# Kernel optimization log

Hardware: AMD Instinct MI355X
Metric: run time of the kernel (lower is better)

The kernel has to match this reference:

```python
import jax, jax.numpy as jnp
import numpy as np

NEG_FILL = -1.0e9
PROB_MIN = 1e-9


def _lstm_cell(x, h, c, w_ih, w_hh, b_ih, b_hh):
    # PyTorch gate order: input, forget, cell(g), output
    gates = x @ w_ih.T + h @ w_hh.T + b_ih + b_hh
    i, f, g, o = jnp.split(gates, 4, axis=-1)
    c_new = jax.nn.sigmoid(f) * c + jax.nn.sigmoid(i) * jnp.tanh(g)
    h_new = jax.nn.sigmoid(o) * jnp.tanh(c_new)
    return h_new, c_new


def setup_inputs() -> dict:
    key = jax.random.key(0)
    B, T, D, H, W = 2048, 100, 128, 256, 256
    ks = jax.random.split(key, 16)
    s_d = 1.0 / np.sqrt(D)
    s_h = 1.0 / np.sqrt(H)
    s_w = 1.0 / np.sqrt(W)
    return {
        "targets": jax.random.normal(ks[0], (B, T, D), jnp.float32),
        "h0": jax.random.normal(ks[1], (1, B, H), jnp.float32),
        "c0": jax.random.normal(ks[2], (1, B, H), jnp.float32),
        "enc_w_ih": jax.random.normal(ks[3], (4 * H, D), jnp.float32) * s_d,
        "enc_w_hh": jax.random.normal(ks[4], (4 * H, H), jnp.float32) * s_h,
        "enc_b_ih": jax.random.normal(ks[5], (4 * H,), jnp.float32) * s_h,
        "enc_b_hh": jax.random.normal(ks[6], (4 * H,), jnp.float32) * s_h,
        "dec_w_ih": jax.random.normal(ks[7], (4 * H, D), jnp.float32) * s_d,
        "dec_w_hh": jax.random.normal(ks[8], (4 * H, H), jnp.float32) * s_h,
        "dec_b_ih": jax.random.normal(ks[9], (4 * H,), jnp.float32) * s_h,
        "dec_b_hh": jax.random.normal(ks[10], (4 * H,), jnp.float32) * s_h,
        "W1": jax.random.normal(ks[11], (W, H), jnp.float32) * s_h,
        "W2": jax.random.normal(ks[12], (W, H), jnp.float32) * s_h,
        "vt": jax.random.normal(ks[13], (W,), jnp.float32) * s_w,
    }


def reference(targets, h0, c0, enc_w_ih, enc_w_hh, enc_b_ih, enc_b_hh,
              dec_w_ih, dec_w_hh, dec_b_ih, dec_b_hh, W1, W2, vt):
    B, T, D = targets.shape
    H = enc_w_hh.shape[1]

    # ---- encoder LSTM (batch_first, zero initial state) ----
    def enc_step(carry, x_t):
        h, c = carry
        h, c = _lstm_cell(x_t, h, c, enc_w_ih, enc_w_hh, enc_b_ih, enc_b_hh)
        return (h, c), h

    z = jnp.zeros((B, H), targets.dtype)
    _, enc_h = jax.lax.scan(enc_step, (z, z), jnp.swapaxes(targets, 0, 1))
    encoder_states = jnp.swapaxes(enc_h, 0, 1)  # [B, T, H]

    blend1 = encoder_states @ W1.T  # [B, T, W]

    a1 = jnp.arange(B)
    init = (h0[0], c0[0], jnp.zeros((B, T), dtype=bool), jnp.zeros_like(targets[:, 0]))

    def dec_step(carry, _):
        h, c, selected, dec_in = carry
        h, c = _lstm_cell(dec_in, h, c, dec_w_ih, dec_w_hh, dec_b_ih, dec_b_hh)
        blend2 = h @ W2.T                                   # [B, W]
        scores = jnp.tanh(blend1 + blend2[:, None, :]) @ vt  # [B, T]
        scores = jnp.where(selected, NEG_FILL, scores)
        sel = jnp.argmax(scores, axis=-1)                    # [B]
        selected = selected.at[a1, sel].set(True)
        probs = jnp.maximum(jax.nn.softmax(scores, axis=-1), PROB_MIN)
        dec_in = targets[a1, sel]                            # [B, D]
        return (h, c, selected, dec_in), probs

    _, probs = jax.lax.scan(dec_step, init, None, length=T)
    return jnp.swapaxes(probs, 0, 1)  # [B, T, T]
```

## Files before the change

### kernel.cpp

```cpp
#include <hip/hip_runtime.h>
#include <math.h>
#include <stdint.h>

#define BB 2048
#define TT 100
#define DD 128
#define HH 256
#define NEGF -1.0e9f

#define NBLK 128
#define ROWS 16
#define NTHR 512
#define KTOT 384
#define NKF  12
#define ASTR 392

typedef __attribute__((ext_vector_type(8))) short short8_t;
typedef __attribute__((ext_vector_type(4))) float f32x4;

#define MFMA16(a,b,c) __builtin_amdgcn_mfma_f32_16x16x32_bf16((a),(b),(c),0,0,0)
#define MFMA_X6(aH,aM,aL,bH,bM,bL,acc)            \
  do{ acc = MFMA16(aM, bM, acc);                  \
      acc = MFMA16(aH, bL, acc);                  \
      acc = MFMA16(aL, bH, acc);                  \
      acc = MFMA16(aH, bM, acc);                  \
      acc = MFMA16(aM, bH, acc);                  \
      acc = MFMA16(aH, bH, acc); }while(0)

__device__ __forceinline__ float sigmoidf_(float x){ return 1.0f/(1.0f+expf(-x)); }

__device__ __forceinline__ float tanh_fast(float x){
  x = fminf(15.f, fmaxf(-15.f, x));
  const float e = __expf(x + x);
  return (e - 1.f) * __builtin_amdgcn_rcpf(e + 1.f);
}

__device__ __forceinline__ void bf16_split3(float x, unsigned short &h,
                                            unsigned short &m, unsigned short &l){
  const unsigned u = __float_as_uint(x);
  const unsigned r = u + 0x7FFFu + ((u >> 16) & 1u);
  h = (unsigned short)(r >> 16);
  const float rem = x - __uint_as_float(r & 0xFFFF0000u);
  const unsigned u2 = __float_as_uint(rem);
  const unsigned r2 = u2 + 0x7FFFu + ((u2 >> 16) & 1u);
  m = (unsigned short)(r2 >> 16);
  const float rem2 = rem - __uint_as_float(r2 & 0xFFFF0000u);
  l = (unsigned short)(__float_as_uint(rem2) >> 16);
}

__global__ __launch_bounds__(256) void k_split3(const float* __restrict__ src,
    unsigned short* __restrict__ hi, unsigned short* __restrict__ mi,
    unsigned short* __restrict__ lo, int n){
  const int i = blockIdx.x*256 + threadIdx.x;
  if(i < n){ unsigned short h,m,l; bf16_split3(src[i], h, m, l);
             hi[i]=h; mi[i]=m; lo[i]=l; }
}

__global__ __launch_bounds__(256) void k_transpose256(const float* __restrict__ in,
                                                      float* __restrict__ outp){
  const int k = blockIdx.x;
  const int n = threadIdx.x;
  outp[k*256 + n] = in[n*256 + k];
}

__global__ __launch_bounds__(256) void k_packW(
    const float* __restrict__ w_ih, const float* __restrict__ w_hh,
    unsigned short* __restrict__ WfH, unsigned short* __restrict__ WfM,
    unsigned short* __restrict__ WfL)
{
  const int i = blockIdx.x*256 + threadIdx.x;
  if(i >= 1024*KTOT) return;
  const int f    = i / (NKF*64*8);
  const int r1   = i % (NKF*64*8);
  const int kf   = r1 >> 9;
  const int r2   = r1 & 511;
  const int lane = r2 >> 3;
  const int e    = r2 & 7;
  const int n = f*16 + (lane & 15);
  const int k = kf*32 + (lane >> 4)*8 + e;
  const float w = (k < DD) ? w_ih[(size_t)n*DD + k] : w_hh[(size_t)n*HH + (k-DD)];
  unsigned short h,m,l; bf16_split3(w,h,m,l);
  WfH[i]=h; WfM[i]=m; WfL[i]=l;
}

__device__ __forceinline__ int swA(int row, int byteoff){
  return row*ASTR + (((byteoff) ^ ((row & 7) << 4)) >> 1);
}

__global__ __launch_bounds__(NTHR) void k_encoder(
    const float* __restrict__ targets,
    const unsigned short* __restrict__ WfH, const unsigned short* __restrict__ WfM,
    const unsigned short* __restrict__ WfL,
    const float* __restrict__ bih, const float* __restrict__ bhh,
    float* __restrict__ blend1)
{
  __shared__ unsigned short AsH[ROWS*ASTR], AsM[ROWS*ASTR], AsL[ROWS*ASTR];
  const int tid = threadIdx.x;
  const int lane = tid & 63;
  const int wv = tid >> 6;
  const int l15 = lane & 15, l4 = lane >> 4;
  const int b0 = blockIdx.x * ROWS;

  float bias[8];
  #pragma unroll
  for(int g=0; g<4; g++)
    #pragma unroll
    for(int c16=0; c16<2; c16++){
      const int n = g*256 + wv*32 + c16*16 + l15;
      bias[g*2+c16] = bih[n] + bhh[n];
    }
  float cst[2][4];
  #pragma unroll
  for(int a=0;a<2;a++)
    #pragma unroll
    for(int r=0;r<4;r++) cst[a][r] = 0.f;

  for(int i=tid; i<ROWS*ASTR; i+=NTHR){ AsH[i]=0; AsM[i]=0; AsL[i]=0; }

  const int srow = tid >> 5;
  const int k4   = (tid & 31) * 4;
  const int sidx = swA(srow, k4*2);

  for(int t=0; t<TT; t++){
    __syncthreads();
    {
      const float4 v = *(const float4*)(targets + ((size_t)(b0+srow)*TT + t)*DD + k4);
      unsigned short h0,m0_,l0,h1,m1_,l1,h2,m2_,l2,h3,m3_,l3;
      bf16_split3(v.x,h0,m0_,l0); bf16_split3(v.y,h1,m1_,l1);
      bf16_split3(v.z,h2,m2_,l2); bf16_split3(v.w,h3,m3_,l3);
      *(ushort4*)&AsH[sidx] = make_ushort4(h0,h1,h2,h3);
      *(ushort4*)&AsM[sidx] = make_ushort4(m0_,m1_,m2_,m3_);
      *(ushort4*)&AsL[sidx] = make_ushort4(l0,l1,l2,l3);
    }
    __syncthreads();
    f32x4 acc[8];
    #pragma unroll
    for(int ff=0; ff<8; ff++){
      acc[ff][0]=bias[ff]; acc[ff][1]=bias[ff]; acc[ff][2]=bias[ff]; acc[ff][3]=bias[ff];
    }
    for(int kf=0; kf<NKF; kf++){
      const int ao = swA(l15, kf*64 + l4*16);
      const short8_t aH = *(const short8_t*)&AsH[ao];
      const short8_t aM = *(const short8_t*)&AsM[ao];
      const short8_t aL = *(const short8_t*)&AsL[ao];
      #pragma unroll
      for(int g=0; g<4; g++)
        #pragma unroll
        for(int c16=0; c16<2; c16++){
          const int f = g*16 + wv*2 + c16;
          const size_t wo = ((size_t)(f*NKF + kf)*64 + lane)*8;
          const short8_t bH = *(const short8_t*)(WfH + wo);
          const short8_t bM = *(const short8_t*)(WfM + wo);
          const short8_t bL = *(const short8_t*)(WfL + wo);
          MFMA_X6(aH,aM,aL,bH,bM,bL, acc[g*2+c16]);
        }
    }
    __syncthreads();
    #pragma unroll
    for(int c16=0; c16<2; c16++){
      const int j = wv*32 + c16*16 + l15;
      #pragma unroll
      for(int r=0; r<4; r++){
        const int row = l4*4 + r;
        const float iv = acc[0+c16][r];
        const float fv = acc[2+c16][r];
        const float gv = acc[4+c16][r];
        const float ov = acc[6+c16][r];
        const float cn = sigmoidf_(fv)*cst[c16][r] + sigmoidf_(iv)*tanhf(gv);
        const float hn = sigmoidf_(ov)*tanhf(cn);
        cst[c16][r] = cn;
        unsigned short sh, sm_, sl;
        bf16_split3(hn, sh, sm_, sl);
        const int hi = swA(row, (128 + j)*2);
        AsH[hi] = sh; AsM[hi] = sm_; AsL[hi] = sl;
        blend1[((size_t)(b0+row)*TT + t)*256 + j] = hn;
      }
    }
  }
}

__global__ __launch_bounds__(NTHR) void k_decoder(
    const float* __restrict__ targets,
    const unsigned short* __restrict__ WfH, const unsigned short* __restrict__ WfM,
    const unsigned short* __restrict__ WfL,
    const float* __restrict__ bih, const float* __restrict__ bhh,
    const float* __restrict__ h0, const float* __restrict__ c0,
    const float* __restrict__ W2t, const float* __restrict__ vt,
    const float* __restrict__ blend1,
    float* __restrict__ outp)
{
  __shared__ unsigned short AsH[ROWS*ASTR], AsM[ROWS*ASTR], AsL[ROWS*ASTR];
  __shared__ float hs[ROWS*264];
  __shared__ float b2s[ROWS*264];
  __shared__ float sc[ROWS][104];
  __shared__ float vts[256];
  __shared__ char selc[ROWS][104];
  const int tid = threadIdx.x;
  const int lane = tid & 63;
  const int wv = tid >> 6;
  const int l15 = lane & 15, l4 = lane >> 4;
  const int b0 = blockIdx.x * ROWS;

  float bias[8];
  #pragma unroll
  for(int g=0; g<4; g++)
    #pragma unroll
    for(int c16=0; c16<2; c16++){
      const int n = g*256 + wv*32 + c16*16 + l15;
      bias[g*2+c16] = bih[n] + bhh[n];
    }

  for(int i=tid; i<ROWS*ASTR; i+=NTHR){ AsH[i]=0; AsM[i]=0; AsL[i]=0; }
  if(tid < 256) vts[tid] = vt[tid];
  for(int i=tid; i<ROWS*104; i+=NTHR) (&selc[0][0])[i] = 0;
  {
    const int row = tid >> 5;
    const int k8  = (tid & 31) * 8;
    #pragma unroll
    for(int ii=0; ii<8; ii+=4){
      const float4 v = *(const float4*)(h0 + (size_t)(b0+row)*HH + k8 + ii);
      unsigned short h0_,m0_,l0,h1,m1_,l1,h2,m2_,l2,h3,m3_,l3;
      bf16_split3(v.x,h0_,m0_,l0); bf16_split3(v.y,h1,m1_,l1);
      bf16_split3(v.z,h2,m2_,l2); bf16_split3(v.w,h3,m3_,l3);
      const int idx = swA(row, (128 + k8 + ii)*2);
      *(ushort4*)&AsH[idx] = make_ushort4(h0_,h1,h2,h3);
      *(ushort4*)&AsM[idx] = make_ushort4(m0_,m1_,m2_,m3_);
      *(ushort4*)&AsL[idx] = make_ushort4(l0,l1,l2,l3);
    }
  }
  float cst[2][4];
  #pragma unroll
  for(int c16=0; c16<2; c16++)
    #pragma unroll
    for(int r=0; r<4; r++)
      cst[c16][r] = c0[(size_t)(b0 + l4*4 + r)*HH + wv*32 + c16*16 + l15];

  for(int st=0; st<TT; st++){
    __syncthreads();
    f32x4 acc[8];
    #pragma unroll
    for(int ff=0; ff<8; ff++){
      acc[ff][0]=bias[ff]; acc[ff][1]=bias[ff]; acc[ff][2]=bias[ff]; acc[ff][3]=bias[ff];
    }
    for(int kf=0; kf<NKF; kf++){
      const int ao = swA(l15, kf*64 + l4*16);
      const short8_t aH = *(const short8_t*)&AsH[ao];
      const short8_t aM = *(const short8_t*)&AsM[ao];
      const short8_t aL = *(const short8_t*)&AsL[ao];
      #pragma unroll
      for(int g=0; g<4; g++)
        #pragma unroll
        for(int c16=0; c16<2; c16++){
          const int f = g*16 + wv*2 + c16;
          const size_t wo = ((size_t)(f*NKF + kf)*64 + lane)*8;
          const short8_t bH = *(const short8_t*)(WfH + wo);
          const short8_t bM = *(const short8_t*)(WfM + wo);
          const short8_t bL = *(const short8_t*)(WfL + wo);
          MFMA_X6(aH,aM,aL,bH,bM,bL, acc[g*2+c16]);
        }
    }
    __syncthreads();
    #pragma unroll
    for(int c16=0; c16<2; c16++){
      const int j = wv*32 + c16*16 + l15;
      #pragma unroll
      for(int r=0; r<4; r++){
        const int row = l4*4 + r;
        const float iv = acc[0+c16][r];
        const float fv = acc[2+c16][r];
        const float gv = acc[4+c16][r];
        const float ov = acc[6+c16][r];
        const float cn = sigmoidf_(fv)*cst[c16][r] + sigmoidf_(iv)*tanhf(gv);
        const float hn = sigmoidf_(ov)*tanhf(cn);
        cst[c16][r] = cn;
        unsigned short sh, sm_, sl;
        bf16_split3(hn, sh, sm_, sl);
        const int hi = swA(row, (128 + j)*2);
        AsH[hi] = sh; AsM[hi] = sm_; AsL[hi] = sl;
        hs[row*264 + j] = hn;
      }
    }
    __syncthreads();
    {
      const int row = tid >> 5;
      const int n8  = (tid & 31) * 8;
      float a8[8];
      #pragma unroll
      for(int i=0;i<8;i++) a8[i] = 0.f;
      #pragma unroll 4
      for(int k=0; k<HH; k++){
        const float hv = hs[row*264 + k];
        const float4 w0 = *(const float4*)(W2t + (size_t)k*HH + n8);
        const float4 w1 = *(const float4*)(W2t + (size_t)k*HH + n8 + 4);
        a8[0]=fmaf(hv,w0.x,a8[0]); a8[1]=fmaf(hv,w0.y,a8[1]);
        a8[2]=fmaf(hv,w0.z,a8[2]); a8[3]=fmaf(hv,w0.w,a8[3]);
        a8[4]=fmaf(hv,w1.x,a8[4]); a8[5]=fmaf(hv,w1.y,a8[5]);
        a8[6]=fmaf(hv,w1.z,a8[6]); a8[7]=fmaf(hv,w1.w,a8[7]);
      }
      #pragma unroll
      for(int i=0;i<8;i++) b2s[row*264 + n8 + i] = a8[i];
    }
    __syncthreads();
    {
      const int g4 = lane >> 4, l16 = lane & 15;
      #pragma unroll
      for(int rr=0; rr<2; rr++){
        const int row = wv*2 + rr;
        const float* bl  = blend1 + ((size_t)(b0+row)*TT)*256;
        const float* b2p = &b2s[row*264];
        for(int tb=0; tb<25; tb++){
          const int t = tb*4 + g4;
          float p = 0.f;
          #pragma unroll
          for(int q=0; q<4; q++){
            const int k = l16*16 + q*4;
            const float4 x   = *(const float4*)(bl + (size_t)t*256 + k);
            const float4 b2v = *(const float4*)(b2p + k);
            const float4 vv4 = *(const float4*)(&vts[k]);
            p = fmaf(tanh_fast(x.x + b2v.x), vv4.x, p);
            p = fmaf(tanh_fast(x.y + b2v.y), vv4.y, p);
            p = fmaf(tanh_fast(x.z + b2v.z), vv4.z, p);
            p = fmaf(tanh_fast(x.w + b2v.w), vv4.w, p);
          }
          #pragma unroll
          for(int off=8; off>=1; off>>=1) p += __shfl_xor(p, off, 64);
          if(l16 == 0) sc[row][t] = p;
        }
      }
    }
    __syncthreads();
    #pragma unroll
    for(int rr=0; rr<2; rr++){
      const int row  = wv*2 + rr;
      const int brow = b0 + row;
      const float m1 = selc[row][lane] ? NEGF : sc[row][lane];
      float bestv = m1; int besti = lane;
      const int t2 = lane + 64;
      float m2 = NEGF;
      if(t2 < TT){
        m2 = selc[row][t2] ? NEGF : sc[row][t2];
        if(m2 > bestv){ bestv = m2; besti = t2; }
      }
      #pragma unroll
      for(int off=32; off>=1; off>>=1){
        const float ov = __shfl_xor(bestv, off, 64);
        const int   oi = __shfl_xor(besti, off, 64);
        if(ov > bestv || (ov == bestv && oi < besti)){ bestv = ov; besti = oi; }
      }
      float e = __expf(m1 - bestv);
      if(t2 < TT) e += __expf(m2 - bestv);
      #pragma unroll
      for(int off=32; off>=1; off>>=1) e += __shfl_xor(e, off, 64);

      float* orow = outp + (size_t)brow*(TT*TT) + (size_t)st*TT;
      orow[lane] = fmaxf(__expf(m1 - bestv)/e, 1e-9f);
      if(t2 < TT) orow[t2] = fmaxf(__expf(m2 - bestv)/e, 1e-9f);
      if(lane == 0) selc[row][besti] = 1;
      #pragma unroll
      for(int dd=0; dd<2; dd++){
        const int d = lane + dd*64;
        const float xv = targets[((size_t)brow*TT + besti)*DD + d];
        unsigned short th, tm, tl;
        bf16_split3(xv, th, tm, tl);
        const int idx = swA(row, d*2);
        AsH[idx] = th; AsM[idx] = tm; AsL[idx] = tl;
      }
    }
  }
}

__global__ __launch_bounds__(128) void k_blend1(
    float* __restrict__ blend1,
    const unsigned short* __restrict__ W1H, const unsigned short* __restrict__ W1M,
    const unsigned short* __restrict__ W1L)
{
  __shared__ alignas(16) unsigned short AsH[32*264], AsM[32*264], AsL[32*264];
  const int tid  = threadIdx.x;
  const int lane = tid & 63;
  const int wv   = tid >> 6;
  const int l15  = lane & 15;
  const int l4   = lane >> 4;
  const size_t r0 = (size_t)blockIdx.x * 32;

  #pragma unroll
  for(int it=0; it<16; it++){
    const int q  = it*128 + tid;
    const int r  = q >> 6;
    const int kq = (q & 63) << 2;
    const float4 v = *(const float4*)(blend1 + (r0+r)*256 + kq);
    unsigned short h0,m0_,l0,h1,m1_,l1,h2,m2_,l2,h3,m3_,l3;
    bf16_split3(v.x,h0,m0_,l0); bf16_split3(v.y,h1,m1_,l1);
    bf16_split3(v.z,h2,m2_,l2); bf16_split3(v.w,h3,m3_,l3);
    *(ushort4*)&AsH[r*264+kq] = make_ushort4(h0,h1,h2,h3);
    *(ushort4*)&AsM[r*264+kq] = make_ushort4(m0_,m1_,m2_,m3_);
    *(ushort4*)&AsL[r*264+kq] = make_ushort4(l0,l1,l2,l3);
  }
  __syncthreads();

  f32x4 acc[16];
  #pragma unroll
  for(int s=0;s<16;s++)
    #pragma unroll
    for(int e=0;e<4;e++) acc[s][e] = 0.f;

  const int rb = wv*16;
  for(int kt=0; kt<8; kt++){
    const int k0 = kt*32;
    const short8_t aH = *(const short8_t*)&AsH[(rb+l15)*264 + k0 + l4*8];
    const short8_t aM = *(const short8_t*)&AsM[(rb+l15)*264 + k0 + l4*8];
    const short8_t aL = *(const short8_t*)&AsL[(rb+l15)*264 + k0 + l4*8];
    #pragma unroll
    for(int fn=0; fn<16; fn++){
      const int n = fn*16 + l15;
      const short8_t bH = *(const short8_t*)(W1H + (size_t)n*256 + k0 + l4*8);
      const short8_t bM = *(const short8_t*)(W1M + (size_t)n*256 + k0 + l4*8);
      const short8_t bL = *(const short8_t*)(W1L + (size_t)n*256 + k0 + l4*8);
      MFMA_X6(aH,aM,aL, bH,bM,bL, acc[fn]);
    }
  }
  #pragma unroll
  for(int fn=0; fn<16; fn++)
    #pragma unroll
    for(int r=0; r<4; r++)
      blend1[(r0 + rb + l4*4 + r)*256 + fn*16 + l15] = acc[fn][r];
}

extern "C" void kernel_launch(void* const* d_in, const int* in_sizes, int n_in,
                              void* d_out, int out_size, void* d_ws, size_t ws_size,
                              hipStream_t stream)
{
  (void)in_sizes; (void)n_in; (void)out_size; (void)ws_size;
  const float* targets  = (const float*)d_in[0];
  const float* h0       = (const float*)d_in[1];
  const float* c0       = (const float*)d_in[2];
  const float* enc_w_ih = (const float*)d_in[3];
  const float* enc_w_hh = (const float*)d_in[4];
  const float* enc_b_ih = (const float*)d_in[5];
  const float* enc_b_hh = (const float*)d_in[6];
  const float* dec_w_ih = (const float*)d_in[7];
  const float* dec_w_hh = (const float*)d_in[8];
  const float* dec_b_ih = (const float*)d_in[9];
  const float* dec_b_hh = (const float*)d_in[10];
  const float* W1       = (const float*)d_in[11];
  const float* W2       = (const float*)d_in[12];
  const float* vt       = (const float*)d_in[13];
  float* outp = (float*)d_out;

  float* ws      = (float*)d_ws;
  float* blend1  = ws;
  float* W2t     = blend1 + (size_t)BB*TT*256;
  char* pc = (char*)(W2t + 256*256);
  pc = (char*)(((uintptr_t)pc + 63) & ~(uintptr_t)63);
  unsigned short* q = (unsigned short*)pc;
  const size_t WFSZ = (size_t)1024*KTOT;
  unsigned short* eWfH = q; q += WFSZ;
  unsigned short* eWfM = q; q += WFSZ;
  unsigned short* eWfL = q; q += WFSZ;
  unsigned short* dWfH = q; q += WFSZ;
  unsigned short* dWfM = q; q += WFSZ;
  unsigned short* dWfL = q; q += WFSZ;
  unsigned short* w1H  = q; q += (size_t)256*256;
  unsigned short* w1M  = q; q += (size_t)256*256;
  unsigned short* w1L  = q; q += (size_t)256*256;

  const int packGrid = (1024*KTOT + 255)/256;
  k_packW<<<packGrid, 256, 0, stream>>>(enc_w_ih, enc_w_hh, eWfH, eWfM, eWfL);
  k_packW<<<packGrid, 256, 0, stream>>>(dec_w_ih, dec_w_hh, dWfH, dWfM, dWfL);
  k_split3<<<(256*256+255)/256, 256, 0, stream>>>(W1, w1H, w1M, w1L, 256*256);
  k_transpose256<<<256, 256, 0, stream>>>(W2, W2t);

  k_encoder<<<NBLK, NTHR, 0, stream>>>(targets, eWfH, eWfM, eWfL,
                                       enc_b_ih, enc_b_hh, blend1);

  k_blend1<<<BB*TT/32, 128, 0, stream>>>(blend1, w1H, w1M, w1L);

  k_decoder<<<NBLK, NTHR, 0, stream>>>(targets, dWfH, dWfM, dWfL,
                                       dec_b_ih, dec_b_hh, h0, c0,
                                       W2t, vt, blend1, outp);
}
```

Measured before the change: 15.94 ms.

## Spread LSTM recurrences over more blocks and move decoder W2 projection to MFMA

The decoder now handles 8 batch rows per block across 256 blocks with 1024 threads, padding the MFMA A tile to 16 rows. The encoder keeps 16 rows per block but uses 1024 threads, so each wave owns one 16-column slice per gate. The scalar fp32 h@W2 loop is replaced by a 3-way bf16-split MFMA against a prepacked W2, and output probabilities are written with nontemporal stores. The intent is to use more CUs and cut per-step latency on the serial recurrence. The cost is wasted MFMA work on the padded rows and more threads contending at each barrier.

```diff
diff --git a/kernel.cpp b/kernel.cpp
--- a/kernel.cpp
+++ b/kernel.cpp
@@ -8,9 +8,10 @@
 #define HH 256
 #define NEGF -1.0e9f
 
-#define NBLK 128
-#define ROWS 16
-#define NTHR 512
+#define NBLK 256
+#define ROWS 8
+#define RA   16
+#define NTHR 1024
 #define KTOT 384
 #define NKF  12
 #define ASTR 392
@@ -54,13 +55,6 @@
   const int i = blockIdx.x*256 + threadIdx.x;
   if(i < n){ unsigned short h,m,l; bf16_split3(src[i], h, m, l);
              hi[i]=h; mi[i]=m; lo[i]=l; }
-}
-
-__global__ __launch_bounds__(256) void k_transpose256(const float* __restrict__ in,
-                                                      float* __restrict__ outp){
-  const int k = blockIdx.x;
-  const int n = threadIdx.x;
-  outp[k*256 + n] = in[n*256 + k];
 }
 
 __global__ __launch_bounds__(256) void k_packW(
@@ -83,6 +77,25 @@
   WfH[i]=h; WfM[i]=m; WfL[i]=l;
 }
 
+__global__ __launch_bounds__(256) void k_packW2(
+    const float* __restrict__ W2,
+    unsigned short* __restrict__ WfH, unsigned short* __restrict__ WfM,
+    unsigned short* __restrict__ WfL)
+{
+  const int i = blockIdx.x*256 + threadIdx.x;
+  if(i >= 256*256) return;
+  const int f2   = i >> 12;
+  const int r1   = i & 4095;
+  const int kf2  = r1 >> 9;
+  const int r2   = r1 & 511;
+  const int lane = r2 >> 3;
+  const int e    = r2 & 7;
+  const int n = f2*16 + (lane & 15);
+  const int k = kf2*32 + (lane >> 4)*8 + e;
+  unsigned short h,m,l; bf16_split3(W2[(size_t)n*HH + k], h, m, l);
+  WfH[i]=h; WfM[i]=m; WfL[i]=l;
+}
+
 __device__ __forceinline__ int swA(int row, int byteoff){
   return row*ASTR + (((byteoff) ^ ((row & 7) << 4)) >> 1);
 }
@@ -94,49 +107,43 @@
     const float* __restrict__ bih, const float* __restrict__ bhh,
     float* __restrict__ blend1)
 {
-  __shared__ unsigned short AsH[ROWS*ASTR], AsM[ROWS*ASTR], AsL[ROWS*ASTR];
+  __shared__ unsigned short AsH[RA*ASTR], AsM[RA*ASTR], AsL[RA*ASTR];
   const int tid = threadIdx.x;
   const int lane = tid & 63;
   const int wv = tid >> 6;
   const int l15 = lane & 15, l4 = lane >> 4;
-  const int b0 = blockIdx.x * ROWS;
-
-  float bias[8];
-  #pragma unroll
-  for(int g=0; g<4; g++)
-    #pragma unroll
-    for(int c16=0; c16<2; c16++){
-      const int n = g*256 + wv*32 + c16*16 + l15;
-      bias[g*2+c16] = bih[n] + bhh[n];
-    }
-  float cst[2][4];
-  #pragma unroll
-  for(int a=0;a<2;a++)
-    #pragma unroll
-    for(int r=0;r<4;r++) cst[a][r] = 0.f;
-
-  for(int i=tid; i<ROWS*ASTR; i+=NTHR){ AsH[i]=0; AsM[i]=0; AsL[i]=0; }
-
-  const int srow = tid >> 5;
-  const int k4   = (tid & 31) * 4;
-  const int sidx = swA(srow, k4*2);
+  const int b0 = blockIdx.x * RA;
+
+  const int j = wv*16 + l15;
+  float bias[4];
+  #pragma unroll
+  for(int g=0; g<4; g++) bias[g] = bih[g*HH + j] + bhh[g*HH + j];
+
+  float cst[4];
+  #pragma unroll
+  for(int r=0;r<4;r++) cst[r] = 0.f;
+
+  for(int i=tid; i<RA*ASTR; i+=NTHR){ AsH[i]=0; AsM[i]=0; AsL[i]=0; }
+
+  const int srow = tid >> 6;
+  const int k2   = (tid & 63) * 2;
 
   for(int t=0; t<TT; t++){
     __syncthreads();
     {
-      const float4 v = *(const float4*)(targets + ((size_t)(b0+srow)*TT + t)*DD + k4);
-      unsigned short h0,m0_,l0,h1,m1_,l1,h2,m2_,l2,h3,m3_,l3;
+      const float2 v = *(const float2*)(targets + ((size_t)(b0+srow)*TT + t)*DD + k2);
+      unsigned short h0,m0_,l0,h1,m1_,l1;
       bf16_split3(v.x,h0,m0_,l0); bf16_split3(v.y,h1,m1_,l1);
-      bf16_split3(v.z,h2,m2_,l2); bf16_split3(v.w,h3,m3_,l3);
-      *(ushort4*)&AsH[sidx] = make_ushort4(h0,h1,h2,h3);
-      *(ushort4*)&AsM[sidx] = make_ushort4(m0_,m1_,m2_,m3_);
-      *(ushort4*)&AsL[sidx] = make_ushort4(l0,l1,l2,l3);
-    }
-    __syncthreads();
-    f32x4 acc[8];
-    #pragma unroll
-    for(int ff=0; ff<8; ff++){
-      acc[ff][0]=bias[ff]; acc[ff][1]=bias[ff]; acc[ff][2]=bias[ff]; acc[ff][3]=bias[ff];
+      const int idx = swA(srow, k2*2);
+      *(ushort2*)&AsH[idx] = make_ushort2(h0,h1);
+      *(ushort2*)&AsM[idx] = make_ushort2(m0_,m1_);
+      *(ushort2*)&AsL[idx] = make_ushort2(l0,l1);
+    }
+    __syncthreads();
+    f32x4 acc[4];
+    #pragma unroll
+    for(int g=0; g<4; g++){
+      acc[g][0]=bias[g]; acc[g][1]=bias[g]; acc[g][2]=bias[g]; acc[g][3]=bias[g];
     }
     for(int kf=0; kf<NKF; kf++){
       const int ao = swA(l15, kf*64 + l4*16);
@@ -144,37 +151,31 @@
       const short8_t aM = *(const short8_t*)&AsM[ao];
       const short8_t aL = *(const short8_t*)&AsL[ao];
       #pragma unroll
-      for(int g=0; g<4; g++)
-        #pragma unroll
-        for(int c16=0; c16<2; c16++){
-          const int f = g*16 + wv*2 + c16;
-          const size_t wo = ((size_t)(f*NKF + kf)*64 + lane)*8;
-          const short8_t bH = *(const short8_t*)(WfH + wo);
-          const short8_t bM = *(const short8_t*)(WfM + wo);
-          const short8_t bL = *(const short8_t*)(WfL + wo);
-          MFMA_X6(aH,aM,aL,bH,bM,bL, acc[g*2+c16]);
-        }
-    }
-    __syncthreads();
-    #pragma unroll
-    for(int c16=0; c16<2; c16++){
-      const int j = wv*32 + c16*16 + l15;
-      #pragma unroll
-      for(int r=0; r<4; r++){
-        const int row = l4*4 + r;
-        const float iv = acc[0+c16][r];
-        const float fv = acc[2+c16][r];
-        const float gv = acc[4+c16][r];
-        const float ov = acc[6+c16][r];
-        const float cn = sigmoidf_(fv)*cst[c16][r] + sigmoidf_(iv)*tanhf(gv);
-        const float hn = sigmoidf_(ov)*tanhf(cn);
-        cst[c16][r] = cn;
-        unsigned short sh, sm_, sl;
-        bf16_split3(hn, sh, sm_, sl);
-        const int hi = swA(row, (128 + j)*2);
-        AsH[hi] = sh; AsM[hi] = sm_; AsL[hi] = sl;
-        blend1[((size_t)(b0+row)*TT + t)*256 + j] = hn;
-      }
+      for(int g=0; g<4; g++){
+        const int f = g*16 + wv;
+        const size_t wo = ((size_t)(f*NKF + kf)*64 + lane)*8;
+        const short8_t bH = *(const short8_t*)(WfH + wo);
+        const short8_t bM = *(const short8_t*)(WfM + wo);
+        const short8_t bL = *(const short8_t*)(WfL + wo);
+        MFMA_X6(aH,aM,aL,bH,bM,bL, acc[g]);
+      }
+    }
+    __syncthreads();
+    #pragma unroll
+    for(int r=0; r<4; r++){
+      const int row = l4*4 + r;
+      const float iv = acc[0][r];
+      const float fv = acc[1][r];
+      const float gv = acc[2][r];
+      const float ov = acc[3][r];
+      const float cn = sigmoidf_(fv)*cst[r] + sigmoidf_(iv)*tanhf(gv);
+      const float hn = sigmoidf_(ov)*tanhf(cn);
+      cst[r] = cn;
+      unsigned short sh, sm_, sl;
+      bf16_split3(hn, sh, sm_, sl);
+      const int hi = swA(row, (128 + j)*2);
+      AsH[hi] = sh; AsM[hi] = sm_; AsL[hi] = sl;
+      blend1[((size_t)(b0+row)*TT + t)*256 + j] = hn;
     }
   }
 }
@@ -183,14 +184,15 @@
     const float* __restrict__ targets,
     const unsigned short* __restrict__ WfH, const unsigned short* __restrict__ WfM,
     const unsigned short* __restrict__ WfL,
+    const unsigned short* __restrict__ W2fH, const unsigned short* __restrict__ W2fM,
+    const unsigned short* __restrict__ W2fL,
     const float* __restrict__ bih, const float* __restrict__ bhh,
     const float* __restrict__ h0, const float* __restrict__ c0,
-    const float* __restrict__ W2t, const float* __restrict__ vt,
+    const float* __restrict__ vt,
     const float* __restrict__ blend1,
     float* __restrict__ outp)
 {
-  __shared__ unsigned short AsH[ROWS*ASTR], AsM[ROWS*ASTR], AsL[ROWS*ASTR];
-  __shared__ float hs[ROWS*264];
+  __shared__ unsigned short AsH[RA*ASTR], AsM[RA*ASTR], AsL[RA*ASTR];
   __shared__ float b2s[ROWS*264];
   __shared__ float sc[ROWS][104];
   __shared__ float vts[256];
@@ -201,46 +203,36 @@
   const int l15 = lane & 15, l4 = lane >> 4;
   const int b0 = blockIdx.x * ROWS;
 
-  float bias[8];
-  #pragma unroll
-  for(int g=0; g<4; g++)
-    #pragma unroll
-    for(int c16=0; c16<2; c16++){
-      const int n = g*256 + wv*32 + c16*16 + l15;
-      bias[g*2+c16] = bih[n] + bhh[n];
-    }
-
-  for(int i=tid; i<ROWS*ASTR; i+=NTHR){ AsH[i]=0; AsM[i]=0; AsL[i]=0; }
+  const int j = wv*16 + l15;
+  float bias[4];
+  #pragma unroll
+  for(int g=0; g<4; g++) bias[g] = bih[g*HH + j] + bhh[g*HH + j];
+
+  for(int i=tid; i<RA*ASTR; i+=NTHR){ AsH[i]=0; AsM[i]=0; AsL[i]=0; }
   if(tid < 256) vts[tid] = vt[tid];
   for(int i=tid; i<ROWS*104; i+=NTHR) (&selc[0][0])[i] = 0;
   {
-    const int row = tid >> 5;
-    const int k8  = (tid & 31) * 8;
-    #pragma unroll
-    for(int ii=0; ii<8; ii+=4){
-      const float4 v = *(const float4*)(h0 + (size_t)(b0+row)*HH + k8 + ii);
-      unsigned short h0_,m0_,l0,h1,m1_,l1,h2,m2_,l2,h3,m3_,l3;
-      bf16_split3(v.x,h0_,m0_,l0); bf16_split3(v.y,h1,m1_,l1);
-      bf16_split3(v.z,h2,m2_,l2); bf16_split3(v.w,h3,m3_,l3);
-      const int idx = swA(row, (128 + k8 + ii)*2);
-      *(ushort4*)&AsH[idx] = make_ushort4(h0_,h1,h2,h3);
-      *(ushort4*)&AsM[idx] = make_ushort4(m0_,m1_,m2_,m3_);
-      *(ushort4*)&AsL[idx] = make_ushort4(l0,l1,l2,l3);
-    }
+    const int row = tid >> 7;
+    const int k2  = (tid & 127) * 2;
+    const float2 v = *(const float2*)(h0 + (size_t)(b0+row)*HH + k2);
+    unsigned short h0_,m0_,l0,h1,m1_,l1;
+    bf16_split3(v.x,h0_,m0_,l0); bf16_split3(v.y,h1,m1_,l1);
+    const int idx = swA(row, (128 + k2)*2);
+    *(ushort2*)&AsH[idx] = make_ushort2(h0_,h1);
+    *(ushort2*)&AsM[idx] = make_ushort2(m0_,m1_);
+    *(ushort2*)&AsL[idx] = make_ushort2(l0,l1);
   }
-  float cst[2][4];
-  #pragma unroll
-  for(int c16=0; c16<2; c16++)
-    #pragma unroll
-    for(int r=0; r<4; r++)
-      cst[c16][r] = c0[(size_t)(b0 + l4*4 + r)*HH + wv*32 + c16*16 + l15];
+  float cst[4];
+  #pragma unroll
+  for(int r=0; r<4; r++)
+    cst[r] = (l4 < 2) ? c0[(size_t)(b0 + l4*4 + r)*HH + j] : 0.f;
 
   for(int st=0; st<TT; st++){
     __syncthreads();
-    f32x4 acc[8];
-    #pragma unroll
-    for(int ff=0; ff<8; ff++){
-      acc[ff][0]=bias[ff]; acc[ff][1]=bias[ff]; acc[ff][2]=bias[ff]; acc[ff][3]=bias[ff];
+    f32x4 acc[4];
+    #pragma unroll
+    for(int g=0; g<4; g++){
+      acc[g][0]=bias[g]; acc[g][1]=bias[g]; acc[g][2]=bias[g]; acc[g][3]=bias[g];
     }
     for(int kf=0; kf<NKF; kf++){
       const int ao = swA(l15, kf*64 + l4*16);
@@ -248,90 +240,89 @@
       const short8_t aM = *(const short8_t*)&AsM[ao];
       const short8_t aL = *(const short8_t*)&AsL[ao];
       #pragma unroll
-      for(int g=0; g<4; g++)
-        #pragma unroll
-        for(int c16=0; c16<2; c16++){
-          const int f = g*16 + wv*2 + c16;
-          const size_t wo = ((size_t)(f*NKF + kf)*64 + lane)*8;
-          const short8_t bH = *(const short8_t*)(WfH + wo);
-          const short8_t bM = *(const short8_t*)(WfM + wo);
-          const short8_t bL = *(const short8_t*)(WfL + wo);
-          MFMA_X6(aH,aM,aL,bH,bM,bL, acc[g*2+c16]);
-        }
-    }
-    __syncthreads();
-    #pragma unroll
-    for(int c16=0; c16<2; c16++){
-      const int j = wv*32 + c16*16 + l15;
+      for(int g=0; g<4; g++){
+        const int f = g*16 + wv;
+        const size_t wo = ((size_t)(f*NKF + kf)*64 + lane)*8;
+        const short8_t bH = *(const short8_t*)(WfH + wo);
+        const short8_t bM = *(const short8_t*)(WfM + wo);
+        const short8_t bL = *(const short8_t*)(WfL + wo);
+        MFMA_X6(aH,aM,aL,bH,bM,bL, acc[g]);
+      }
+    }
+    __syncthreads();
+    if(l4 < 2){
       #pragma unroll
       for(int r=0; r<4; r++){
         const int row = l4*4 + r;
-        const float iv = acc[0+c16][r];
-        const float fv = acc[2+c16][r];
-        const float gv = acc[4+c16][r];
-        const float ov = acc[6+c16][r];
-        const float cn = sigmoidf_(fv)*cst[c16][r] + sigmoidf_(iv)*tanhf(gv);
+        const float iv = acc[0][r];
+        const float fv = acc[1][r];
+        const float gv = acc[2][r];
+        const float ov = acc[3][r];
+        const float cn = sigmoidf_(fv)*cst[r] + sigmoidf_(iv)*tanhf(gv);
         const float hn = sigmoidf_(ov)*tanhf(cn);
-        cst[c16][r] = cn;
+        cst[r] = cn;
         unsigned short sh, sm_, sl;
         bf16_split3(hn, sh, sm_, sl);
         const int hi = swA(row, (128 + j)*2);
         AsH[hi] = sh; AsM[hi] = sm_; AsL[hi] = sl;
-        hs[row*264 + j] = hn;
       }
     }
     __syncthreads();
     {
-      const int row = tid >> 5;
-      const int n8  = (tid & 31) * 8;
-      float a8[8];
-      #pragma unroll
-      for(int i=0;i<8;i++) a8[i] = 0.f;
-      #pragma unroll 4
-      for(int k=0; k<HH; k++){
-        const float hv = hs[row*264 + k];
-        const float4 w0 = *(const float4*)(W2t + (size_t)k*HH + n8);
-        const float4 w1 = *(const float4*)(W2t + (size_t)k*HH + n8 + 4);
-        a8[0]=fmaf(hv,w0.x,a8[0]); a8[1]=fmaf(hv,w0.y,a8[1]);
-        a8[2]=fmaf(hv,w0.z,a8[2]); a8[3]=fmaf(hv,w0.w,a8[3]);
-        a8[4]=fmaf(hv,w1.x,a8[4]); a8[5]=fmaf(hv,w1.y,a8[5]);
-        a8[6]=fmaf(hv,w1.z,a8[6]); a8[7]=fmaf(hv,w1.w,a8[7]);
-      }
-      #pragma unroll
-      for(int i=0;i<8;i++) b2s[row*264 + n8 + i] = a8[i];
+      f32x4 b2acc;
+      b2acc[0]=0.f; b2acc[1]=0.f; b2acc[2]=0.f; b2acc[3]=0.f;
+      for(int kf2=0; kf2<8; kf2++){
+        const int ao = swA(l15, (kf2+4)*64 + l4*16);
+        const short8_t aH = *(const short8_t*)&AsH[ao];
+        const short8_t aM = *(const short8_t*)&AsM[ao];
+        const short8_t aL = *(const short8_t*)&AsL[ao];
+        const size_t wo = ((size_t)(wv*8 + kf2)*64 + lane)*8;
+        const short8_t bH = *(const short8_t*)(W2fH + wo);
+        const short8_t bM = *(const short8_t*)(W2fM + wo);
+        const short8_t bL = *(const short8_t*)(W2fL + wo);
+        MFMA_X6(aH,aM,aL,bH,bM,bL, b2acc);
+      }
+      if(l4 < 2){
+        #pragma unroll
+        for(int r=0; r<4; r++)
+          b2s[(l4*4 + r)*264 + wv*16 + l15] = b2acc[r];
+      }
     }
     __syncthreads();
     {
+      const int row = wv >> 1;
+      const int tb0 = wv & 1;
       const int g4 = lane >> 4, l16 = lane & 15;
-      #pragma unroll
-      for(int rr=0; rr<2; rr++){
-        const int row = wv*2 + rr;
-        const float* bl  = blend1 + ((size_t)(b0+row)*TT)*256;
-        const float* b2p = &b2s[row*264];
-        for(int tb=0; tb<25; tb++){
+      const float* bl  = blend1 + (size_t)(b0+row)*TT*256;
+      const float* b2p = &b2s[row*264];
+      #pragma unroll
+      for(int i=0; i<13; i++){
+        const int tb = tb0 + 2*i;
+        if(tb < 25){
           const int t = tb*4 + g4;
           float p = 0.f;
           #pragma unroll
           for(int q=0; q<4; q++){
-            const int k = l16*16 + q*4;
+            const int k = q*64 + l16*4;
             const float4 x   = *(const float4*)(bl + (size_t)t*256 + k);
-            const float4 b2v = *(const float4*)(b2p + k);
+            const float4 bv  = *(const float4*)(b2p + k);
             const float4 vv4 = *(const float4*)(&vts[k]);
-            p = fmaf(tanh_fast(x.x + b2v.x), vv4.x, p);
-            p = fmaf(tanh_fast(x.y + b2v.y), vv4.y, p);
-            p = fmaf(tanh_fast(x.z + b2v.z), vv4.z, p);
-            p = fmaf(tanh_fast(x.w + b2v.w), vv4.w, p);
+            p = fmaf(tanh_fast(x.x + bv.x), vv4.x, p);
+            p = fmaf(tanh_fast(x.y + bv.y), vv4.y, p);
+            p = fmaf(tanh_fast(x.z + bv.z), vv4.z, p);
+            p = fmaf(tanh_fast(x.w + bv.w), vv4.w, p);
           }
-          #pragma unroll
-          for(int off=8; off>=1; off>>=1) p += __shfl_xor(p, off, 64);
+          p += __shfl_xor(p, 8, 64);
+          p += __shfl_xor(p, 4, 64);
+          p += __shfl_xor(p, 2, 64);
+          p += __shfl_xor(p, 1, 64);
           if(l16 == 0) sc[row][t] = p;
         }
       }
     }
     __syncthreads();
-    #pragma unroll
-    for(int rr=0; rr<2; rr++){
-      const int row  = wv*2 + rr;
+    if(wv < ROWS){
+      const int row  = wv;
       const int brow = b0 + row;
       const float m1 = selc[row][lane] ? NEGF : sc[row][lane];
       float bestv = m1; int besti = lane;
@@ -353,8 +344,9 @@
       for(int off=32; off>=1; off>>=1) e += __shfl_xor(e, off, 64);
 
       float* orow = outp + (size_t)brow*(TT*TT) + (size_t)st*TT;
-      orow[lane] = fmaxf(__expf(m1 - bestv)/e, 1e-9f);
-      if(t2 < TT) orow[t2] = fmaxf(__expf(m2 - bestv)/e, 1e-9f);
+      __builtin_nontemporal_store(fmaxf(__expf(m1 - bestv)/e, 1e-9f), orow + lane);
+      if(t2 < TT)
+        __builtin_nontemporal_store(fmaxf(__expf(m2 - bestv)/e, 1e-9f), orow + t2);
       if(lane == 0) selc[row][besti] = 1;
       #pragma unroll
       for(int dd=0; dd<2; dd++){
@@ -448,8 +440,7 @@
 
   float* ws      = (float*)d_ws;
   float* blend1  = ws;
-  float* W2t     = blend1 + (size_t)BB*TT*256;
-  char* pc = (char*)(W2t + 256*256);
+  char* pc = (char*)(blend1 + (size_t)BB*TT*256);
   pc = (char*)(((uintptr_t)pc + 63) & ~(uintptr_t)63);
   unsigned short* q = (unsigned short*)pc;
   const size_t WFSZ = (size_t)1024*KTOT;
@@ -459,6 +450,9 @@
   unsigned short* dWfH = q; q += WFSZ;
   unsigned short* dWfM = q; q += WFSZ;
   unsigned short* dWfL = q; q += WFSZ;
+  unsigned short* w2fH = q; q += (size_t)256*256;
+  unsigned short* w2fM = q; q += (size_t)256*256;
+  unsigned short* w2fL = q; q += (size_t)256*256;
   unsigned short* w1H  = q; q += (size_t)256*256;
   unsigned short* w1M  = q; q += (size_t)256*256;
   unsigned short* w1L  = q; q += (size_t)256*256;
@@ -466,15 +460,16 @@
   const int packGrid = (1024*KTOT + 255)/256;
   k_packW<<<packGrid, 256, 0, stream>>>(enc_w_ih, enc_w_hh, eWfH, eWfM, eWfL);
   k_packW<<<packGrid, 256, 0, stream>>>(dec_w_ih, dec_w_hh, dWfH, dWfM, dWfL);
+  k_packW2<<<(256*256+255)/256, 256, 0, stream>>>(W2, w2fH, w2fM, w2fL);
   k_split3<<<(256*256+255)/256, 256, 0, stream>>>(W1, w1H, w1M, w1L, 256*256);
-  k_transpose256<<<256, 256, 0, stream>>>(W2, W2t);
-
-  k_encoder<<<NBLK, NTHR, 0, stream>>>(targets, eWfH, eWfM, eWfL,
-                                       enc_b_ih, enc_b_hh, blend1);
+
+  k_encoder<<<BB/RA, NTHR, 0, stream>>>(targets, eWfH, eWfM, eWfL,
+                                        enc_b_ih, enc_b_hh, blend1);
 
   k_blend1<<<BB*TT/32, 128, 0, stream>>>(blend1, w1H, w1M, w1L);
 
   k_decoder<<<NBLK, NTHR, 0, stream>>>(targets, dWfH, dWfM, dWfL,
+                                       w2fH, w2fM, w2fL,
                                        dec_b_ih, dec_b_hh, h0, c0,
-                                       W2t, vt, blend1, outp);
-}
+                                       vt, blend1, outp);
+}
```

New measurement: 30.05 ms. 88.5% more time.
